# Kernel tuning notes

Hardware: AMD Instinct MI355X
Metric: run time of the kernel (lower is better)

Reference implementation:

```python
import jax, jax.numpy as jnp
import numpy as np

N_SPARSE = 26
VOCAB = 50000
EMB_DIM = 64
DENSE_DIM = 13
INPUT_DIM = N_SPARSE * EMB_DIM + DENSE_DIM  # 1677
HIDDEN = [1024, 512, 256]
N_CROSS = 3
BATCH = 16384
EPS = 1e-5


def setup_inputs() -> dict:
    key = jax.random.key(0)
    ks = jax.random.split(key, 24)
    inp = {}
    inp["sparse_data"] = jax.random.randint(ks[0], (BATCH, N_SPARSE), 0, VOCAB, dtype=jnp.int64 if jax.config.jax_enable_x64 else jnp.int32)
    inp["dense_data"] = jax.random.normal(ks[1], (BATCH, DENSE_DIM), dtype=jnp.float32)
    # stacked embedding tables [F, V, E] (nn.Embedding default init N(0,1); scaled down for stability)
    inp["emb_tables"] = jax.random.normal(ks[2], (N_SPARSE, VOCAB, EMB_DIM), dtype=jnp.float32) * 0.1
    # cross layers: Linear(input_dim, 1) per layer -> weight [L, D], bias [L]
    inp["w_cross"] = jax.random.normal(ks[3], (N_CROSS, INPUT_DIM), dtype=jnp.float32) * 0.02
    inp["b_cross"] = jnp.zeros((N_CROSS,), dtype=jnp.float32)
    # deep tower
    inp["bn0_g"] = jnp.ones((INPUT_DIM,), jnp.float32); inp["bn0_b"] = jnp.zeros((INPUT_DIM,), jnp.float32)
    inp["W1"] = jax.random.normal(ks[4], (INPUT_DIM, HIDDEN[0]), jnp.float32) * 0.02
    inp["bias1"] = jnp.zeros((HIDDEN[0],), jnp.float32)
    inp["bn1_g"] = jnp.ones((HIDDEN[0],), jnp.float32); inp["bn1_b"] = jnp.zeros((HIDDEN[0],), jnp.float32)
    inp["W2"] = jax.random.normal(ks[5], (HIDDEN[0], HIDDEN[1]), jnp.float32) * 0.02
    inp["bias2"] = jnp.zeros((HIDDEN[1],), jnp.float32)
    inp["bn2_g"] = jnp.ones((HIDDEN[1],), jnp.float32); inp["bn2_b"] = jnp.zeros((HIDDEN[1],), jnp.float32)
    inp["W3"] = jax.random.normal(ks[6], (HIDDEN[1], HIDDEN[2]), jnp.float32) * 0.02
    inp["bias3"] = jnp.zeros((HIDDEN[2],), jnp.float32)
    inp["bn3_g"] = jnp.ones((HIDDEN[2],), jnp.float32); inp["bn3_b"] = jnp.zeros((HIDDEN[2],), jnp.float32)
    # predict: Linear(hidden[-1] + input_dim, 1)
    inp["Wp"] = jax.random.normal(ks[7], (HIDDEN[2] + INPUT_DIM, 1), jnp.float32) * 0.02
    inp["bp"] = jnp.zeros((1,), jnp.float32)
    return inp


def _bn(x, g, b):
    # BatchNorm1d, training mode: biased batch stats over batch dim
    mu = jnp.mean(x, axis=0)
    var = jnp.mean((x - mu) ** 2, axis=0)
    return g * (x - mu) * jax.lax.rsqrt(var + EPS) + b


def reference(sparse_data, dense_data, emb_tables, w_cross, b_cross,
              bn0_g, bn0_b, W1, bias1, bn1_g, bn1_b, W2, bias2, bn2_g, bn2_b,
              W3, bias3, bn3_g, bn3_b, Wp, bp):
    # --- embedding (faithful to source bug: column 0 is used for every feature) ---
    idx0 = sparse_data[:, 0]                         # [B]
    emb = emb_tables[:, idx0, :]                     # [F, B, E]
    emb = jnp.transpose(emb, (1, 0, 2)).reshape(idx0.shape[0], -1)  # [B, F*E]

    x0 = jnp.concatenate([emb, dense_data], axis=1)  # [B, D]

    # --- cross network: Linear_i(x0^T x0) + x0 == x0*(x0@w_i) + b_i + x0 ---
    # (source restarts from cross_input each iteration, so only last layer matters;
    #  loop kept for fidelity, it is cheap)
    cross = x0
    for i in range(N_CROSS):
        s = x0 @ w_cross[i]                          # [B]
        cross = x0 * s[:, None] + b_cross[i] + x0    # [B, D]

    # --- deep tower: BN -> (Linear -> Dropout(eval=id) -> BN) x3, no activations ---
    h = _bn(x0, bn0_g, bn0_b)
    h = _bn(h @ W1 + bias1, bn1_g, bn1_b)
    h = _bn(h @ W2 + bias2, bn2_g, bn2_b)
    h = _bn(h @ W3 + bias3, bn3_g, bn3_b)

    out = jnp.concatenate([cross, h], axis=1) @ Wp + bp  # [B, 1]
    return jax.nn.sigmoid(out)
```

## Files before the change

kernel.cpp:

```cpp
#include <hip/hip_runtime.h>
#include <hip/hip_bf16.h>
#include <cstdint>
#include <cstddef>

#define AS1 __attribute__((address_space(1)))
#define AS3 __attribute__((address_space(3)))

typedef __attribute__((ext_vector_type(8))) short short8v;
typedef __attribute__((ext_vector_type(4))) float f32x4;
typedef unsigned short u16;

constexpr int kBatch = 16384;
constexpr int kNSp   = 26;
constexpr int kVocab = 50000;
constexpr int kEmb   = 64;
constexpr int kInDim = 1677;
constexpr int kInPad = 1728;
constexpr int kDense = 13;
constexpr int kH1 = 1024, kH2 = 512, kH3 = 256;
constexpr float kEps = 1e-5f;

__device__ __forceinline__ float b2f(u16 s) {
  unsigned u = ((unsigned)s) << 16;
  union { unsigned u; float f; } c; c.u = u; return c.f;
}
__device__ __forceinline__ u16 f2b(float f) {
  __hip_bfloat16 h = __float2bfloat16(f);
  return __builtin_bit_cast(u16, h);
}

__global__ void prep_kernel(const float* __restrict__ Wp, float* __restrict__ misc) {
  __shared__ float red[256];
  float s = 0.f;
  for (int j = threadIdx.x; j < kInDim; j += 256) s += Wp[j];
  red[threadIdx.x] = s;
  __syncthreads();
  for (int k = 128; k > 0; k >>= 1) {
    if (threadIdx.x < k) red[threadIdx.x] += red[threadIdx.x + k];
    __syncthreads();
  }
  if (threadIdx.x == 0) misc[0] = red[0];
}

__global__ void gather_kernel(const int* __restrict__ sparse, const float* __restrict__ dense,
                              const float* __restrict__ emb, const float* __restrict__ w_cross,
                              const float* __restrict__ b_cross, const float* __restrict__ Wp,
                              const float* __restrict__ misc, u16* __restrict__ x0,
                              float* __restrict__ crossc) {
  const int b = blockIdx.x;
  const int tid = threadIdx.x;
  const int idx = sparse[b * kNSp];
  const float* wc2 = w_cross + 2 * kInDim;
  u16* xrow = x0 + (size_t)b * kInPad;
  float u = 0.f, v = 0.f;
  for (int q = tid; q < 416; q += 256) {
    int p = q * 4;
    const float* src = emb + ((size_t)(p >> 6) * kVocab + idx) * kEmb + (p & 63);
    float4 val = *(const float4*)src;
    u += val.x * wc2[p] + val.y * wc2[p + 1] + val.z * wc2[p + 2] + val.w * wc2[p + 3];
    v += val.x * Wp[p]  + val.y * Wp[p + 1]  + val.z * Wp[p + 2]  + val.w * Wp[p + 3];
    ushort4 o;
    o.x = f2b(val.x); o.y = f2b(val.y); o.z = f2b(val.z); o.w = f2b(val.w);
    *(ushort4*)(xrow + p) = o;
  }
  int p = 1664 + tid;
  if (p < kInPad) {
    float val = 0.f;
    if (p < kInDim) {
      val = dense[b * kDense + (p - 1664)];
      u += val * wc2[p];
      v += val * Wp[p];
    }
    xrow[p] = f2b(val);
  }
  #pragma unroll
  for (int off = 32; off; off >>= 1) {
    u += __shfl_down(u, off, 64);
    v += __shfl_down(v, off, 64);
  }
  __shared__ float su[4], sv[4];
  int lane = tid & 63, wv = tid >> 6;
  if (lane == 0) { su[wv] = u; sv[wv] = v; }
  __syncthreads();
  if (tid == 0) {
    float uu = su[0] + su[1] + su[2] + su[3];
    float vv = sv[0] + sv[1] + sv[2] + sv[3];
    crossc[b] = (1.f + uu) * vv + b_cross[2] * misc[0];
  }
}

__global__ void colstats_kernel(const u16* __restrict__ X, int ld, int rpb,
                                float* __restrict__ sum, float* __restrict__ sq) {
  int c  = threadIdx.x & 63;
  int rg = threadIdx.x >> 6;
  int col = blockIdx.x * 64 + c;
  int r0  = blockIdx.y * rpb;
  float s = 0.f, s2 = 0.f;
  for (int r = r0 + rg; r < r0 + rpb; r += 4) {
    float v = b2f(X[(size_t)r * ld + col]);
    s += v; s2 += v * v;
  }
  __shared__ float sh[8][64];
  sh[rg][c] = s; sh[rg + 4][c] = s2;
  __syncthreads();
  if (rg == 0) atomicAdd(&sum[col], sh[0][c] + sh[1][c] + sh[2][c] + sh[3][c]);
  else if (rg == 1) atomicAdd(&sq[col], sh[4][c] + sh[5][c] + sh[6][c] + sh[7][c]);
}

__global__ void fold_kernel(const float* __restrict__ W, const float* __restrict__ sum,
                            const float* __restrict__ sq, const float* __restrict__ g,
                            const float* __restrict__ bb, float invM,
                            u16* __restrict__ Wt, float* __restrict__ bfold,
                            int K, int N, int Kp) {
  __shared__ float t[64][65];
  int kb = blockIdx.x * 64;
  int nb = blockIdx.y * 64;
  int c  = threadIdx.x & 63;
  int r0 = threadIdx.x >> 6;
  #pragma unroll
  for (int rr = 0; rr < 64; rr += 4) {
    int k = kb + rr + r0;
    t[rr + r0][c] = (k < K) ? W[(size_t)k * N + nb + c] : 0.f;
  }
  __syncthreads();
  int k = kb + c;
  float a = 0.f, cc = 0.f;
  if (k < K) {
    float mu  = sum[k] * invM;
    float var = sq[k] * invM - mu * mu;
    a  = g[k] * rsqrtf(var + kEps);
    cc = bb[k] - a * mu;
  }
  #pragma unroll
  for (int rr = 0; rr < 64; rr += 4) {
    int n = nb + rr + r0;
    float w = t[c][rr + r0];
    Wt[(size_t)n * Kp + k] = f2b(w * a);
    float part = cc * w;
    #pragma unroll
    for (int off = 32; off; off >>= 1) part += __shfl_xor(part, off, 64);
    if (c == 0) atomicAdd(&bfold[n], part);
  }
}

__global__ __launch_bounds__(256) void gemm_kernel(
    const u16* __restrict__ A, const u16* __restrict__ Bt,
    const float* __restrict__ bias, const float* __restrict__ bfold,
    u16* __restrict__ Z, float* __restrict__ sum, float* __restrict__ sq,
    int M, int N, int Kp) {
  __shared__ char lds[32768];
  char* ldsA = lds;
  char* ldsB = lds + 16384;
  const int tid  = threadIdx.x;
  const int lane = tid & 63;
  const int wv   = tid >> 6;
  const int wr = wv >> 1, wc = wv & 1;
  const int r16 = lane & 15, kg = lane >> 4;

  const int L   = blockIdx.y * gridDim.x + blockIdx.x;
  const int xcd = L & 7;
  const int j   = L >> 3;
  const int mb  = xcd * 16 + (j & 15);
  const int nb  = j >> 4;
  const int m0 = mb * 128;
  const int n0 = nb * 128;
  const int ldb = Kp * 2;

  const char* gA = (const char*)A + (size_t)m0 * ldb;
  const char* gB = (const char*)Bt + (size_t)n0 * ldb;

  const char* srcA[4]; const char* srcB[4]; int dst[4];
  #pragma unroll
  for (int rr = 0; rr < 4; ++rr) {
    int lb  = (rr * 256 + tid) * 16;
    int row = lb >> 7;
    int kb  = lb & 127;
    int kbs = kb ^ ((row & 7) << 4);
    dst[rr]  = lb;
    srcA[rr] = gA + (size_t)row * ldb + kbs;
    srcB[rr] = gB + (size_t)row * ldb + kbs;
  }

  f32x4 acc[4][4];
  #pragma unroll
  for (int m = 0; m < 4; ++m)
    #pragma unroll
    for (int n = 0; n < 4; ++n) acc[m][n] = (f32x4){0.f, 0.f, 0.f, 0.f};

  for (int k0 = 0; k0 < Kp; k0 += 64) {
    __syncthreads();
    #pragma unroll
    for (int rr = 0; rr < 4; ++rr)
      __builtin_amdgcn_global_load_lds((const AS1 unsigned*)(srcA[rr] + k0 * 2),
                                       (AS3 unsigned*)(ldsA + dst[rr]), 16, 0, 0);
    #pragma unroll
    for (int rr = 0; rr < 4; ++rr)
      __builtin_amdgcn_global_load_lds((const AS1 unsigned*)(srcB[rr] + k0 * 2),
                                       (AS3 unsigned*)(ldsB + dst[rr]), 16, 0, 0);
    asm volatile("s_waitcnt vmcnt(0)" ::: "memory");
    __syncthreads();
    #pragma unroll
    for (int kk = 0; kk < 2; ++kk) {
      short8v av[4], bv[4];
      #pragma unroll
      for (int m = 0; m < 4; ++m) {
        int row = wr * 64 + m * 16 + r16;
        int kb  = (kk * 64 + kg * 16) ^ ((row & 7) << 4);
        av[m] = *(const short8v*)(ldsA + row * 128 + kb);
      }
      #pragma unroll
      for (int n = 0; n < 4; ++n) {
        int row = wc * 64 + n * 16 + r16;
        int kb  = (kk * 64 + kg * 16) ^ ((row & 7) << 4);
        bv[n] = *(const short8v*)(ldsB + row * 128 + kb);
      }
      #pragma unroll
      for (int m = 0; m < 4; ++m)
        #pragma unroll
        for (int n = 0; n < 4; ++n)
          acc[m][n] = __builtin_amdgcn_mfma_f32_16x16x32_bf16(av[m], bv[n], acc[m][n], 0, 0, 0);
    }
  }
  #pragma unroll
  for (int n = 0; n < 4; ++n) {
    int col = n0 + wc * 64 + n * 16 + r16;
    float bs = bias[col] + bfold[col];
    float ps = 0.f, pq = 0.f;
    #pragma unroll
    for (int m = 0; m < 4; ++m) {
      int rbase = m0 + wr * 64 + m * 16 + kg * 4;
      #pragma unroll
      for (int j2 = 0; j2 < 4; ++j2) {
        float val = acc[m][n][j2] + bs;
        Z[(size_t)(rbase + j2) * N + col] = f2b(val);
        ps += val; pq += val * val;
      }
    }
    ps += __shfl_xor(ps, 16, 64); ps += __shfl_xor(ps, 32, 64);
    pq += __shfl_xor(pq, 16, 64); pq += __shfl_xor(pq, 32, 64);
    if (lane < 16) {
      atomicAdd(&sum[col], ps);
      atomicAdd(&sq[col],  pq);
    }
  }
}


#define STAGE(OP, H, TILE)                                                      \
  {                                                                             \
    const char* sb = ((OP) ? gB : gA) + (size_t)((H) * 128) * ldb               \
                     + (size_t)(TILE) * 128 + srcoff;                           \
    char* db = lds + (((TILE) & 1) << 16) + ((OP) << 15) + ((H) << 14) + tid * 16; \
    __builtin_amdgcn_global_load_lds((const AS1 unsigned*)sb,                   \
                                     (AS3 unsigned*)db, 16, 0, 0);              \
    __builtin_amdgcn_global_load_lds((const AS1 unsigned*)(sb + 64 * (size_t)ldb), \
                                     (AS3 unsigned*)(db + 8192), 16, 0, 0);     \
  }

#define PHASE(T, MH, NH)                                                        \
  {                                                                             \
    char* la  = lds + (((T) & 1) << 16);                                        \
    char* lbp = la + 32768;                                                     \
    short8v av[4][2], bv[2][2];                                                 \
    _Pragma("unroll")                                                           \
    for (int fm = 0; fm < 4; ++fm) {                                            \
      int row = (MH) * 128 + wr * 64 + fm * 16 + r16;                           \
      _Pragma("unroll")                                                         \
      for (int kk = 0; kk < 2; ++kk) {                                          \
        int kb = (kk * 64 + kg * 16) ^ ((row & 7) << 4);                        \
        av[fm][kk] = *(const short8v*)(la + row * 128 + kb);                    \
      }                                                                         \
    }                                                                           \
    _Pragma("unroll")                                                           \
    for (int fn = 0; fn < 2; ++fn) {                                            \
      int row = (NH) * 128 + wc * 32 + fn * 16 + r16;                           \
      _Pragma("unroll")                                                         \
      for (int kk = 0; kk < 2; ++kk) {                                          \
        int kb = (kk * 64 + kg * 16) ^ ((row & 7) << 4);                        \
        bv[fn][kk] = *(const short8v*)(lbp + row * 128 + kb);                   \
      }                                                                         \
    }                                                                           \
    __builtin_amdgcn_s_setprio(1);                                              \
    _Pragma("unroll")                                                           \
    for (int fm = 0; fm < 4; ++fm)                                              \
      _Pragma("unroll")                                                         \
      for (int fn = 0; fn < 2; ++fn)                                            \
        _Pragma("unroll")                                                       \
        for (int kk = 0; kk < 2; ++kk)                                          \
          acc[(MH) * 4 + fm][(NH) * 2 + fn] =                                   \
              __builtin_amdgcn_mfma_f32_16x16x32_bf16(                          \
                  av[fm][kk], bv[fn][kk],                                       \
                  acc[(MH) * 4 + fm][(NH) * 2 + fn], 0, 0, 0);                  \
    __builtin_amdgcn_s_setprio(0);                                              \
  }

#define BAR_VM8()                                                               \
  {                                                                             \
    asm volatile("s_waitcnt vmcnt(8)" ::: "memory");                            \
    __builtin_amdgcn_sched_barrier(0);                                          \
    __builtin_amdgcn_s_barrier();                                               \
    __builtin_amdgcn_sched_barrier(0);                                          \
  }
#define BAR_VM0()                                                               \
  {                                                                             \
    asm volatile("s_waitcnt vmcnt(0)" ::: "memory");                            \
    __builtin_amdgcn_sched_barrier(0);                                          \
    __builtin_amdgcn_s_barrier();                                               \
    __builtin_amdgcn_sched_barrier(0);                                          \
  }
#define BAR_NOVM()                                                              \
  {                                                                             \
    __builtin_amdgcn_sched_barrier(0);                                          \
    __builtin_amdgcn_s_barrier();                                               \
    __builtin_amdgcn_sched_barrier(0);                                          \
  }

__global__ __launch_bounds__(512, 2) void gemm256_kernel(
    const u16* __restrict__ A, const u16* __restrict__ Bt,
    const float* __restrict__ bias, const float* __restrict__ bfold,
    u16* __restrict__ Z, float* __restrict__ sum, float* __restrict__ sq,
    int M, int N, int Kp) {
  __shared__ char lds[131072];
  const int tid  = threadIdx.x;
  const int lane = tid & 63;
  const int wid  = tid >> 6;
  const int wr = wid >> 2, wc = wid & 3;
  const int r16 = lane & 15, kg = lane >> 4;

  const int nmb = M >> 8;
  const int cpx = nmb >> 3;
  const int L   = blockIdx.x;
  const int xcd = L & 7;
  const int jj  = L >> 3;
  const int mb  = xcd * cpx + (jj % cpx);
  const int nb  = jj / cpx;
  const int m0  = mb * 256;
  const int n0  = nb * 256;
  const int ldb = Kp * 2;
  const int nt  = Kp >> 6;

  const char* gA = (const char*)A + (size_t)m0 * ldb;
  const char* gB = (const char*)Bt + (size_t)n0 * ldb;
  const int row0 = tid >> 3;
  const int kbs  = ((tid & 7) * 16) ^ ((row0 & 7) << 4);
  const size_t srcoff = (size_t)row0 * ldb + kbs;

  f32x4 acc[8][4];
  #pragma unroll
  for (int m = 0; m < 8; ++m)
    #pragma unroll
    for (int n = 0; n < 4; ++n) acc[m][n] = (f32x4){0.f, 0.f, 0.f, 0.f};

  STAGE(0, 0, 0); STAGE(1, 0, 0); STAGE(1, 1, 0); STAGE(0, 1, 0);
  STAGE(0, 0, 1); STAGE(1, 0, 1);
  BAR_VM8();

  const int Tmain = nt - 2;
  for (int T = 0; T < Tmain; ++T) {
    STAGE(1, 1, T + 1);
    PHASE(T, 0, 0);
    BAR_VM8();
    STAGE(0, 1, T + 1);
    PHASE(T, 0, 1);
    BAR_VM8();
    if (T + 2 < nt) STAGE(0, 0, T + 2);
    PHASE(T, 1, 0);
    BAR_NOVM();
    if (T + 2 < nt) STAGE(1, 0, T + 2);
    PHASE(T, 1, 1);
    BAR_VM8();
  }
  for (int T = Tmain; T < nt; ++T) {
    if (T + 1 < nt) STAGE(1, 1, T + 1);
    PHASE(T, 0, 0);
    BAR_VM0();
    if (T + 1 < nt) STAGE(0, 1, T + 1);
    PHASE(T, 0, 1);
    BAR_VM0();
    PHASE(T, 1, 0);
    BAR_NOVM();
    PHASE(T, 1, 1);
    BAR_VM0();
  }

  #pragma unroll
  for (int nh = 0; nh < 2; ++nh)
    #pragma unroll
    for (int fn = 0; fn < 2; ++fn) {
      int col = n0 + nh * 128 + wc * 32 + fn * 16 + r16;
      float bs = bias[col] + bfold[col];
      float ps = 0.f, pq = 0.f;
      #pragma unroll
      for (int mh = 0; mh < 2; ++mh)
        #pragma unroll
        for (int fm = 0; fm < 4; ++fm) {
          int rbase = m0 + mh * 128 + wr * 64 + fm * 16 + kg * 4;
          #pragma unroll
          for (int j2 = 0; j2 < 4; ++j2) {
            float val = acc[mh * 4 + fm][nh * 2 + fn][j2] + bs;
            Z[(size_t)(rbase + j2) * N + col] = f2b(val);
            ps += val; pq += val * val;
          }
        }
      ps += __shfl_xor(ps, 16, 64); ps += __shfl_xor(ps, 32, 64);
      pq += __shfl_xor(pq, 16, 64); pq += __shfl_xor(pq, 32, 64);
      if (lane < 16) {
        atomicAdd(&sum[col], ps);
        atomicAdd(&sq[col],  pq);
      }
    }
}

__global__ void final_kernel(const u16* __restrict__ z3, const float* __restrict__ sum3,
                             const float* __restrict__ sq3, const float* __restrict__ g3,
                             const float* __restrict__ b3, float invM,
                             const float* __restrict__ Wp, const float* __restrict__ bp,
                             const float* __restrict__ crossc, float* __restrict__ out) {
  int wv = threadIdx.x >> 6, lane = threadIdx.x & 63;
  int b = blockIdx.x * 4 + wv;
  const float* wph = Wp + kInDim;
  float s = 0.f;
  #pragma unroll
  for (int k = lane; k < kH3; k += 64) {
    float mu  = sum3[k] * invM;
    float var = sq3[k] * invM - mu * mu;
    float a   = g3[k] * rsqrtf(var + kEps);
    float cc  = b3[k] - a * mu;
    float h = a * b2f(z3[(size_t)b * kH3 + k]) + cc;
    s += h * wph[k];
  }
  #pragma unroll
  for (int off = 32; off; off >>= 1) s += __shfl_down(s, off, 64);
  if (lane == 0) {
    float logit = s + crossc[b] + bp[0];
    out[b] = 1.f / (1.f + expf(-logit));
  }
}

constexpr size_t OFF_X0    = 0;
constexpr size_t OFF_Z1    = OFF_X0 + (size_t)kBatch * kInPad * 2;
constexpr size_t OFF_Z2    = OFF_Z1 + (size_t)kBatch * kH1 * 2;
constexpr size_t OFF_Z3    = OFF_Z2 + (size_t)kBatch * kH2 * 2;
constexpr size_t OFF_W1T   = OFF_Z3 + (size_t)kBatch * kH3 * 2;
constexpr size_t OFF_W2T   = OFF_W1T + (size_t)kH1 * kInPad * 2;
constexpr size_t OFF_W3T   = OFF_W2T + (size_t)kH2 * kH1 * 2;
constexpr size_t OFF_CROSS = OFF_W3T + (size_t)kH3 * kH2 * 2;
constexpr size_t OFF_STATS = OFF_CROSS + (size_t)kBatch * 4;
constexpr size_t STATS_FLOATS = 2 * (kInPad + kH1 + kH2 + kH3);
constexpr size_t BF_FLOATS = kH1 + kH2 + kH3;
constexpr size_t OFF_BF    = OFF_STATS + STATS_FLOATS * 4;
constexpr size_t OFF_MISC  = OFF_BF + BF_FLOATS * 4;

extern "C" void kernel_launch(void* const* d_in, const int* in_sizes, int n_in,
                              void* d_out, int out_size, void* d_ws, size_t ws_size,
                              hipStream_t stream) {
  const int*   sparse  = (const int*)d_in[0];
  const float* dense   = (const float*)d_in[1];
  const float* emb     = (const float*)d_in[2];
  const float* w_cross = (const float*)d_in[3];
  const float* b_cross = (const float*)d_in[4];
  const float* bn0_g = (const float*)d_in[5],  *bn0_b = (const float*)d_in[6];
  const float* W1    = (const float*)d_in[7],  *bias1 = (const float*)d_in[8];
  const float* bn1_g = (const float*)d_in[9],  *bn1_b = (const float*)d_in[10];
  const float* W2    = (const float*)d_in[11], *bias2 = (const float*)d_in[12];
  const float* bn2_g = (const float*)d_in[13], *bn2_b = (const float*)d_in[14];
  const float* W3    = (const float*)d_in[15], *bias3 = (const float*)d_in[16];
  const float* bn3_g = (const float*)d_in[17], *bn3_b = (const float*)d_in[18];
  const float* Wp    = (const float*)d_in[19], *bp    = (const float*)d_in[20];

  char* ws = (char*)d_ws;
  u16* x0  = (u16*)(ws + OFF_X0);
  u16* z1  = (u16*)(ws + OFF_Z1);
  u16* z2  = (u16*)(ws + OFF_Z2);
  u16* z3  = (u16*)(ws + OFF_Z3);
  u16* W1t = (u16*)(ws + OFF_W1T);
  u16* W2t = (u16*)(ws + OFF_W2T);
  u16* W3t = (u16*)(ws + OFF_W3T);
  float* crossc = (float*)(ws + OFF_CROSS);
  float* stats  = (float*)(ws + OFF_STATS);
  float* sum0 = stats,            *sq0 = stats + kInPad;
  float* sum1 = sq0 + kInPad,     *sq1 = sum1 + kH1;
  float* sum2 = sq1 + kH1,        *sq2 = sum2 + kH2;
  float* sum3 = sq2 + kH2,        *sq3 = sum3 + kH3;
  float* bfold = (float*)(ws + OFF_BF);
  float* b1f = bfold, *b2f = b1f + kH1, *b3f = b2f + kH2;
  float* misc = (float*)(ws + OFF_MISC);
  float* out = (float*)d_out;

  const float invM = 1.f / (float)kBatch;

  hipMemsetAsync(stats, 0, (STATS_FLOATS + BF_FLOATS) * 4, stream);
  prep_kernel<<<1, 256, 0, stream>>>(Wp, misc);

  gather_kernel<<<kBatch, 256, 0, stream>>>(sparse, dense, emb, w_cross, b_cross, Wp, misc,
                                            x0, crossc);

  colstats_kernel<<<dim3(kInPad / 64, 32), 256, 0, stream>>>(x0, kInPad, kBatch / 32, sum0, sq0);
  fold_kernel<<<dim3(kInPad / 64, kH1 / 64), 256, 0, stream>>>(
      W1, sum0, sq0, bn0_g, bn0_b, invM, W1t, b1f, kInDim, kH1, kInPad);

  gemm256_kernel<<<(kBatch / 256) * (kH1 / 256), 512, 0, stream>>>(
      x0, W1t, bias1, b1f, z1, sum1, sq1, kBatch, kH1, kInPad);
  fold_kernel<<<dim3(kH1 / 64, kH2 / 64), 256, 0, stream>>>(
      W2, sum1, sq1, bn1_g, bn1_b, invM, W2t, b2f, kH1, kH2, kH1);

  gemm_kernel<<<dim3(kH2 / 128, kBatch / 128), 256, 0, stream>>>(
      z1, W2t, bias2, b2f, z2, sum2, sq2, kBatch, kH2, kH1);
  fold_kernel<<<dim3(kH2 / 64, kH3 / 64), 256, 0, stream>>>(
      W3, sum2, sq2, bn2_g, bn2_b, invM, W3t, b3f, kH2, kH3, kH2);

  gemm_kernel<<<dim3(kH3 / 128, kBatch / 128), 256, 0, stream>>>(
      z2, W3t, bias3, b3f, z3, sum3, sq3, kBatch, kH3, kH2);

  final_kernel<<<kBatch / 4, 256, 0, stream>>>(z3, sum3, sq3, bn3_g, bn3_b, invM,
                                               Wp, bp, crossc, out);
}
```

Baseline: 237.2 us.

## Add pipelined 256x128 GEMM kernel for layer 2 and fold stats zeroing into prep

Adds a new 512-thread 256x128-tile GEMM for the second layer. It uses direct global-to-LDS loads, double-buffered A and B tiles, XCD-aware block mapping and an interleaved wait/barrier schedule, replacing the older 128x128 gemm_kernel there. The hipMemsetAsync that zeroed the stats buffers is removed and the zeroing moves into the single-block prep kernel, saving one launch. The barrier macros are generalized into BAR_VMN(N). The risks are lower occupancy from the 96KB LDS footprint and a serial zeroing loop in a single block.

```diff
diff --git a/kernel.cpp b/kernel.cpp
--- a/kernel.cpp
+++ b/kernel.cpp
@@ -20,6 +20,9 @@
 constexpr int kH1 = 1024, kH2 = 512, kH3 = 256;
 constexpr float kEps = 1e-5f;
 
+constexpr int kStatsFloats = 2 * (kInPad + kH1 + kH2 + kH3);
+constexpr int kBfFloats    = kH1 + kH2 + kH3;
+
 __device__ __forceinline__ float b2f(u16 s) {
   unsigned u = ((unsigned)s) << 16;
   union { unsigned u; float f; } c; c.u = u; return c.f;
@@ -29,7 +32,9 @@
   return __builtin_bit_cast(u16, h);
 }
 
-__global__ void prep_kernel(const float* __restrict__ Wp, float* __restrict__ misc) {
+__global__ void prep_kernel(const float* __restrict__ Wp, float* __restrict__ stats,
+                            float* __restrict__ misc) {
+  for (int i = threadIdx.x; i < kStatsFloats + kBfFloats; i += 256) stats[i] = 0.f;
   __shared__ float red[256];
   float s = 0.f;
   for (int j = threadIdx.x; j < kInDim; j += 256) s += Wp[j];
@@ -244,6 +249,20 @@
     }
   }
 }
+
+#define BAR_VMN(N)                                                              \
+  {                                                                             \
+    asm volatile("s_waitcnt vmcnt(" #N ")" ::: "memory");                       \
+    __builtin_amdgcn_sched_barrier(0);                                          \
+    __builtin_amdgcn_s_barrier();                                               \
+    __builtin_amdgcn_sched_barrier(0);                                          \
+  }
+#define BAR_NOVM()                                                              \
+  {                                                                             \
+    __builtin_amdgcn_sched_barrier(0);                                          \
+    __builtin_amdgcn_s_barrier();                                               \
+    __builtin_amdgcn_sched_barrier(0);                                          \
+  }
 
 
 #define STAGE(OP, H, TILE)                                                      \
@@ -294,27 +313,6 @@
     __builtin_amdgcn_s_setprio(0);                                              \
   }
 
-#define BAR_VM8()                                                               \
-  {                                                                             \
-    asm volatile("s_waitcnt vmcnt(8)" ::: "memory");                            \
-    __builtin_amdgcn_sched_barrier(0);                                          \
-    __builtin_amdgcn_s_barrier();                                               \
-    __builtin_amdgcn_sched_barrier(0);                                          \
-  }
-#define BAR_VM0()                                                               \
-  {                                                                             \
-    asm volatile("s_waitcnt vmcnt(0)" ::: "memory");                            \
-    __builtin_amdgcn_sched_barrier(0);                                          \
-    __builtin_amdgcn_s_barrier();                                               \
-    __builtin_amdgcn_sched_barrier(0);                                          \
-  }
-#define BAR_NOVM()                                                              \
-  {                                                                             \
-    __builtin_amdgcn_sched_barrier(0);                                          \
-    __builtin_amdgcn_s_barrier();                                               \
-    __builtin_amdgcn_sched_barrier(0);                                          \
-  }
-
 __global__ __launch_bounds__(512, 2) void gemm256_kernel(
     const u16* __restrict__ A, const u16* __restrict__ Bt,
     const float* __restrict__ bias, const float* __restrict__ bfold,
@@ -353,34 +351,34 @@
 
   STAGE(0, 0, 0); STAGE(1, 0, 0); STAGE(1, 1, 0); STAGE(0, 1, 0);
   STAGE(0, 0, 1); STAGE(1, 0, 1);
-  BAR_VM8();
+  BAR_VMN(8);
 
   const int Tmain = nt - 2;
   for (int T = 0; T < Tmain; ++T) {
     STAGE(1, 1, T + 1);
     PHASE(T, 0, 0);
-    BAR_VM8();
+    BAR_VMN(8);
     STAGE(0, 1, T + 1);
     PHASE(T, 0, 1);
-    BAR_VM8();
+    BAR_VMN(8);
     if (T + 2 < nt) STAGE(0, 0, T + 2);
     PHASE(T, 1, 0);
     BAR_NOVM();
     if (T + 2 < nt) STAGE(1, 0, T + 2);
     PHASE(T, 1, 1);
-    BAR_VM8();
+    BAR_VMN(8);
   }
   for (int T = Tmain; T < nt; ++T) {
     if (T + 1 < nt) STAGE(1, 1, T + 1);
     PHASE(T, 0, 0);
-    BAR_VM0();
+    BAR_VMN(0);
     if (T + 1 < nt) STAGE(0, 1, T + 1);
     PHASE(T, 0, 1);
-    BAR_VM0();
+    BAR_VMN(0);
     PHASE(T, 1, 0);
     BAR_NOVM();
     PHASE(T, 1, 1);
-    BAR_VM0();
+    BAR_VMN(0);
   }
 
   #pragma unroll
@@ -411,6 +409,141 @@
     }
 }
 
+
+#define STAGE2A(H, TILE)                                                        \
+  {                                                                             \
+    const char* sb = gA + (size_t)((H) * 128) * ldb + (size_t)(TILE) * 128 + srcoff; \
+    char* db = lds + (((TILE) & 1) << 15) + ((H) << 14) + tid * 16;             \
+    __builtin_amdgcn_global_load_lds((const AS1 unsigned*)sb,                   \
+                                     (AS3 unsigned*)db, 16, 0, 0);              \
+    __builtin_amdgcn_global_load_lds((const AS1 unsigned*)(sb + 64 * (size_t)ldb), \
+                                     (AS3 unsigned*)(db + 8192), 16, 0, 0);     \
+  }
+#define STAGE2B(TILE)                                                           \
+  {                                                                             \
+    const char* sb = gB + (size_t)(TILE) * 128 + srcoff;                        \
+    char* db = lds + 65536 + (((TILE) & 1) << 14) + tid * 16;                   \
+    __builtin_amdgcn_global_load_lds((const AS1 unsigned*)sb,                   \
+                                     (AS3 unsigned*)db, 16, 0, 0);              \
+    __builtin_amdgcn_global_load_lds((const AS1 unsigned*)(sb + 64 * (size_t)ldb), \
+                                     (AS3 unsigned*)(db + 8192), 16, 0, 0);     \
+  }
+
+#define PHASE2(T, MH)                                                           \
+  {                                                                             \
+    char* la  = lds + (((T) & 1) << 15) + ((MH) << 14);                         \
+    char* lbp = lds + 65536 + (((T) & 1) << 14);                                \
+    short8v av[4][2], bv[2][2];                                                 \
+    _Pragma("unroll")                                                           \
+    for (int fm = 0; fm < 4; ++fm) {                                            \
+      int row = wr * 64 + fm * 16 + r16;                                        \
+      _Pragma("unroll")                                                         \
+      for (int kk = 0; kk < 2; ++kk) {                                          \
+        int kb = (kk * 64 + kg * 16) ^ ((row & 7) << 4);                        \
+        av[fm][kk] = *(const short8v*)(la + row * 128 + kb);                    \
+      }                                                                         \
+    }                                                                           \
+    _Pragma("unroll")                                                           \
+    for (int fn = 0; fn < 2; ++fn) {                                            \
+      int row = wc * 32 + fn * 16 + r16;                                        \
+      _Pragma("unroll")                                                         \
+      for (int kk = 0; kk < 2; ++kk) {                                          \
+        int kb = (kk * 64 + kg * 16) ^ ((row & 7) << 4);                        \
+        bv[fn][kk] = *(const short8v*)(lbp + row * 128 + kb);                   \
+      }                                                                         \
+    }                                                                           \
+    __builtin_amdgcn_s_setprio(1);                                              \
+    _Pragma("unroll")                                                           \
+    for (int fm = 0; fm < 4; ++fm)                                              \
+      _Pragma("unroll")                                                         \
+      for (int fn = 0; fn < 2; ++fn)                                            \
+        _Pragma("unroll")                                                       \
+        for (int kk = 0; kk < 2; ++kk)                                          \
+          acc[(MH) * 4 + fm][fn] =                                              \
+              __builtin_amdgcn_mfma_f32_16x16x32_bf16(                          \
+                  av[fm][kk], bv[fn][kk], acc[(MH) * 4 + fm][fn], 0, 0, 0);     \
+    __builtin_amdgcn_s_setprio(0);                                              \
+  }
+
+__global__ __launch_bounds__(512, 2) void gemm256x128_kernel(
+    const u16* __restrict__ A, const u16* __restrict__ Bt,
+    const float* __restrict__ bias, const float* __restrict__ bfold,
+    u16* __restrict__ Z, float* __restrict__ sum, float* __restrict__ sq,
+    int M, int N, int Kp) {
+  __shared__ char lds[98304];
+  const int tid  = threadIdx.x;
+  const int lane = tid & 63;
+  const int wid  = tid >> 6;
+  const int wr = wid >> 2, wc = wid & 3;
+  const int r16 = lane & 15, kg = lane >> 4;
+
+  const int nmb = M >> 8;
+  const int cpx = nmb >> 3;
+  const int L   = blockIdx.x;
+  const int xcd = L & 7;
+  const int jj  = L >> 3;
+  const int mb  = xcd * cpx + (jj % cpx);
+  const int nb  = jj / cpx;
+  const int m0  = mb * 256;
+  const int n0  = nb * 128;
+  const int ldb = Kp * 2;
+  const int nt  = Kp >> 6;
+
+  const char* gA = (const char*)A + (size_t)m0 * ldb;
+  const char* gB = (const char*)Bt + (size_t)n0 * ldb;
+  const int row0 = tid >> 3;
+  const int kbs  = ((tid & 7) * 16) ^ ((row0 & 7) << 4);
+  const size_t srcoff = (size_t)row0 * ldb + kbs;
+
+  f32x4 acc[8][2];
+  #pragma unroll
+  for (int m = 0; m < 8; ++m)
+    #pragma unroll
+    for (int n = 0; n < 2; ++n) acc[m][n] = (f32x4){0.f, 0.f, 0.f, 0.f};
+
+  STAGE2A(0, 0); STAGE2B(0); STAGE2A(1, 0);
+
+  const int Tmain = nt - 1;
+  for (int T = 0; T < Tmain; ++T) {
+    STAGE2A(0, T + 1); STAGE2B(T + 1);
+    BAR_VMN(6);
+    PHASE2(T, 0);
+    STAGE2A(1, T + 1);
+    BAR_VMN(6);
+    PHASE2(T, 1);
+    BAR_NOVM();
+  }
+  BAR_VMN(2);
+  PHASE2(nt - 1, 0);
+  BAR_VMN(0);
+  PHASE2(nt - 1, 1);
+
+  #pragma unroll
+  for (int fn = 0; fn < 2; ++fn) {
+    int col = n0 + wc * 32 + fn * 16 + r16;
+    float bs = bias[col] + bfold[col];
+    float ps = 0.f, pq = 0.f;
+    #pragma unroll
+    for (int mh = 0; mh < 2; ++mh)
+      #pragma unroll
+      for (int fm = 0; fm < 4; ++fm) {
+        int rbase = m0 + mh * 128 + wr * 64 + fm * 16 + kg * 4;
+        #pragma unroll
+        for (int j2 = 0; j2 < 4; ++j2) {
+          float val = acc[mh * 4 + fm][fn][j2] + bs;
+          Z[(size_t)(rbase + j2) * N + col] = f2b(val);
+          ps += val; pq += val * val;
+        }
+      }
+    ps += __shfl_xor(ps, 16, 64); ps += __shfl_xor(ps, 32, 64);
+    pq += __shfl_xor(pq, 16, 64); pq += __shfl_xor(pq, 32, 64);
+    if (lane < 16) {
+      atomicAdd(&sum[col], ps);
+      atomicAdd(&sq[col],  pq);
+    }
+  }
+}
+
 __global__ void final_kernel(const u16* __restrict__ z3, const float* __restrict__ sum3,
                              const float* __restrict__ sq3, const float* __restrict__ g3,
                              const float* __restrict__ b3, float invM,
@@ -446,10 +579,8 @@
 constexpr size_t OFF_W3T   = OFF_W2T + (size_t)kH2 * kH1 * 2;
 constexpr size_t OFF_CROSS = OFF_W3T + (size_t)kH3 * kH2 * 2;
 constexpr size_t OFF_STATS = OFF_CROSS + (size_t)kBatch * 4;
-constexpr size_t STATS_FLOATS = 2 * (kInPad + kH1 + kH2 + kH3);
-constexpr size_t BF_FLOATS = kH1 + kH2 + kH3;
-constexpr size_t OFF_BF    = OFF_STATS + STATS_FLOATS * 4;
-constexpr size_t OFF_MISC  = OFF_BF + BF_FLOATS * 4;
+constexpr size_t OFF_BF    = OFF_STATS + (size_t)kStatsFloats * 4;
+constexpr size_t OFF_MISC  = OFF_BF + (size_t)kBfFloats * 4;
 
 extern "C" void kernel_launch(void* const* d_in, const int* in_sizes, int n_in,
                               void* d_out, int out_size, void* d_ws, size_t ws_size,
@@ -489,8 +620,7 @@
 
   const float invM = 1.f / (float)kBatch;
 
-  hipMemsetAsync(stats, 0, (STATS_FLOATS + BF_FLOATS) * 4, stream);
-  prep_kernel<<<1, 256, 0, stream>>>(Wp, misc);
+  prep_kernel<<<1, 256, 0, stream>>>(Wp, stats, misc);
 
   gather_kernel<<<kBatch, 256, 0, stream>>>(sparse, dense, emb, w_cross, b_cross, Wp, misc,
                                             x0, crossc);
@@ -504,7 +634,7 @@
   fold_kernel<<<dim3(kH1 / 64, kH2 / 64), 256, 0, stream>>>(
       W2, sum1, sq1, bn1_g, bn1_b, invM, W2t, b2f, kH1, kH2, kH1);
 
-  gemm_kernel<<<dim3(kH2 / 128, kBatch / 128), 256, 0, stream>>>(
+  gemm256x128_kernel<<<(kBatch / 256) * (kH2 / 128), 512, 0, stream>>>(
       z1, W2t, bias2, b2f, z2, sum2, sq2, kBatch, kH2, kH1);
   fold_kernel<<<dim3(kH2 / 64, kH3 / 64), 256, 0, stream>>>(
       W3, sum2, sq2, bn2_g, bn2_b, invM, W3t, b3f, kH2, kH3, kH2);
```

Result: faster. 227.7 us (-4.0%).
